# Performance work log

Hardware: AMD Instinct MI355X
Metric: run time of the kernel (lower is better)

The kernel has to match this reference:

```python
import jax, jax.numpy as jnp
import numpy as np

N = 10000      # num_nodes
F = 4          # node_features (in_channels)
P = 12         # periods
OUT = 256      # out_channels
HID = 128      # hidden_dim
ODIM = 12      # output_dim
E_MAIN = 160000
E_REG = 40000


def setup_inputs() -> dict:
    key = jax.random.key(0)
    ks = jax.random.split(key, 48)
    d = {}
    d["x"] = jax.random.normal(ks[0], (N, F, P), jnp.float32)
    d["edge_index"] = jax.random.randint(ks[1], (2, E_MAIN), 0, N)
    names = ["IA", "KS", "KY", "OH", "WI"]
    for i, nm in enumerate(names):
        d[f"edge_{nm}_index"] = jax.random.randint(ks[2 + i], (2, E_REG), 0, N)
        d[f"edge_{nm}_weight"] = jax.random.uniform(ks[7 + i], (E_REG,), jnp.float32)
    def w(k, shape, fan_in):
        return jax.random.normal(k, shape, jnp.float32) * (1.0 / np.sqrt(fan_in))
    # ChebConv K=2 (shared across 5 regions)
    d["cheb_W0"] = w(ks[12], (F, OUT), F)
    d["cheb_W1"] = w(ks[13], (F, OUT), F)
    d["cheb_b"] = jnp.zeros((OUT,), jnp.float32)
    # concat linear 5*OUT -> OUT
    d["lin_cat_W"] = w(ks[14], (5 * OUT, OUT), 5 * OUT)
    d["lin_cat_b"] = jnp.zeros((OUT,), jnp.float32)
    # per-period attention logits
    d["attention"] = jax.random.uniform(ks[15], (P,), jnp.float32)
    # TGCN gates: GCNConv weights + linears
    d["gz_W"] = w(ks[16], (F, OUT), F); d["gz_b"] = jnp.zeros((OUT,), jnp.float32)
    d["gr_W"] = w(ks[17], (F, OUT), F); d["gr_b"] = jnp.zeros((OUT,), jnp.float32)
    d["gh_W"] = w(ks[18], (F, OUT), F); d["gh_b"] = jnp.zeros((OUT,), jnp.float32)
    d["lz_W"] = w(ks[19], (2 * OUT, OUT), 2 * OUT); d["lz_b"] = jnp.ones((OUT,), jnp.float32)
    d["lr_W"] = w(ks[20], (2 * OUT, OUT), 2 * OUT); d["lr_b"] = jnp.ones((OUT,), jnp.float32)
    d["lh_W"] = w(ks[21], (2 * OUT, OUT), 2 * OUT); d["lh_b"] = jnp.ones((OUT,), jnp.float32)
    # readout head
    d["out1_W"] = w(ks[22], (OUT, HID), OUT); d["out1_b"] = jnp.zeros((HID,), jnp.float32)
    d["out2_W"] = w(ks[23], (HID, ODIM), HID); d["out2_b"] = jnp.zeros((ODIM,), jnp.float32)
    return d


def _cheb(x, ei, ew, W0, W1, b):
    # PyG ChebConv, K=2, sym norm, lambda_max=2 => Tx1 = -D^{-1/2} A D^{-1/2} x
    src, dst = ei[0], ei[1]
    deg = jax.ops.segment_sum(ew, src, num_segments=N)
    dinv = jnp.where(deg > 0, jax.lax.rsqrt(jnp.maximum(deg, 1e-12)), 0.0)
    norm = dinv[src] * ew * dinv[dst]                    # [E]
    Tx1 = -jax.ops.segment_sum(norm[:, None] * x[src], dst, num_segments=N)
    return x @ W0 + Tx1 @ W1 + b


def _gcn(x, ei, W, b):
    # PyG GCNConv, edge_weight=None, add_self_loops=True
    xw = x @ W                                           # [N, OUT]
    src, dst = ei[0], ei[1]
    deg = jax.ops.segment_sum(jnp.ones((ei.shape[1],), xw.dtype), dst,
                              num_segments=N) + 1.0      # +1 self loop
    dinv = jax.lax.rsqrt(deg)
    norm = dinv[src] * dinv[dst]                         # [E]
    agg = jax.ops.segment_sum(norm[:, None] * xw[src], dst, num_segments=N)
    agg = agg + (dinv * dinv)[:, None] * xw              # self-loop term
    return agg + b


def _forward(x, edge_index, reg_idx, reg_w,
             cheb_W0, cheb_W1, cheb_b, lin_cat_W, lin_cat_b, attention,
             gz_W, gz_b, gr_W, gr_b, gh_W, gh_b,
             lz_W, lz_b, lr_W, lr_b, lh_W, lh_b,
             out1_W, out1_b, out2_W, out2_b):
    probs = jax.nn.softmax(attention)
    H_accum = jnp.zeros((N, OUT), x.dtype)
    for p in range(P):
        Xp = x[:, :, p]                                  # [N, F]
        hs = jnp.concatenate(
            [_cheb(Xp, ri, rw, cheb_W0, cheb_W1, cheb_b)
             for ri, rw in zip(reg_idx, reg_w)], axis=1)  # [N, 5*OUT]
        h = jax.nn.leaky_relu(hs @ lin_cat_W + lin_cat_b, 0.01)  # [N, OUT]
        # TGCN cell with H = h
        Z = jax.nn.sigmoid(jnp.concatenate([_gcn(Xp, edge_index, gz_W, gz_b), h], 1) @ lz_W + lz_b)
        R = jax.nn.sigmoid(jnp.concatenate([_gcn(Xp, edge_index, gr_W, gr_b), h], 1) @ lr_W + lr_b)
        Ht = jnp.tanh(jnp.concatenate([_gcn(Xp, edge_index, gh_W, gh_b), h * R], 1) @ lh_W + lh_b)
        Hp = Z * h + (1.0 - Z) * Ht
        H_accum = H_accum + probs[p] * Hp
    out_hidden = H_accum
    hr = jax.nn.relu(H_accum)
    o = jax.nn.relu(hr @ out1_W + out1_b) @ out2_W + out2_b  # [N, ODIM]
    return o, out_hidden


def reference(x, edge_index, edge_IA_index, edge_KS_index, edge_KY_index,
              edge_OH_index, edge_WI_index, edge_IA_weight, edge_KS_weight,
              edge_KY_weight, edge_OH_weight, edge_WI_weight,
              cheb_W0, cheb_W1, cheb_b, lin_cat_W, lin_cat_b, attention,
              gz_W, gz_b, gr_W, gr_b, gh_W, gh_b,
              lz_W, lz_b, lr_W, lr_b, lh_W, lh_b,
              out1_W, out1_b, out2_W, out2_b):
    reg_idx = (edge_IA_index, edge_KS_index, edge_KY_index, edge_OH_index, edge_WI_index)
    reg_w = (edge_IA_weight, edge_KS_weight, edge_KY_weight, edge_OH_weight, edge_WI_weight)
    return _forward(x, edge_index, reg_idx, reg_w,
                    cheb_W0, cheb_W1, cheb_b, lin_cat_W, lin_cat_b, attention,
                    gz_W, gz_b, gr_W, gr_b, gh_W, gh_b,
                    lz_W, lz_b, lr_W, lr_b, lh_W, lh_b,
                    out1_W, out1_b, out2_W, out2_b)
```

## Files before the change

kernel.cpp:

```cpp
#include <hip/hip_runtime.h>
#include <hip/hip_bf16.h>
#include <cstddef>

#define NN    10000
#define PP    12
#define EMAIN 160000
#define EREG  40000
#define OUTD  256
#define HIDD  128

typedef __attribute__((ext_vector_type(8))) short bf16x8;
typedef __attribute__((ext_vector_type(4))) float f32x4;

enum : int {
  WS_PROBS    = 0,
  WS_DEGM     = 16,
  WS_DEGR     = WS_DEGM + NN,
  WS_AGGM     = WS_DEGR + 5 * NN,
  WS_TX1      = WS_AGGM + NN * 48,
  WS_ZERO_END = WS_TX1 + 5 * NN * 48,
  WS_DINVM    = WS_ZERO_END,
  WS_DINV2M   = WS_DINVM + NN,
  WS_DINVR    = WS_DINV2M + NN,
  WS_NORMM    = WS_DINVR + 5 * NN,
  WS_NORMR    = WS_NORMM + EMAIN,
  WS_MCAT     = WS_NORMR + 5 * EREG,
  WS_BIASH    = WS_MCAT + 24 * OUTD,
  WS_AZ       = WS_BIASH + OUTD,
  WS_AR       = WS_AZ + 4 * OUTD,
  WS_AH       = WS_AR + 4 * OUTD,
  WS_BZ       = WS_AH + 4 * OUTD,
  WS_BR       = WS_BZ + OUTD,
  WS_BH       = WS_BR + OUTD,
  WS_MCT      = WS_BH + OUTD,
  WS_WZT      = WS_MCT + 4096,
  WS_WRT      = WS_WZT + 36864,
  WS_WHT      = WS_WRT + 36864,
  WS_TOTAL    = WS_WHT + 36864
};

__device__ __forceinline__ float sigm(float v) { return 1.f / (1.f + __expf(-v)); }
__device__ __forceinline__ float tanh_f(float v) { float e = __expf(2.f * v); return 1.f - 2.f / (e + 1.f); }

__device__ __forceinline__ short bf16c(float v) {
  __hip_bfloat16 h = __float2bfloat16(v);
  short r;
  __builtin_memcpy(&r, &h, sizeof(r));
  return r;
}
__device__ __forceinline__ unsigned cvt2(float a, float b) {
  __hip_bfloat162 h2 = __float22bfloat162_rn(make_float2(a, b));
  unsigned r;
  __builtin_memcpy(&r, &h2, sizeof(r));
  return r;
}
__device__ __forceinline__ float upk_lo(unsigned u) { return __uint_as_float(u << 16); }
__device__ __forceinline__ float upk_hi(unsigned u) { return __uint_as_float(u & 0xffff0000u); }

__device__ __forceinline__ const int* sel_i(int r, const int* a, const int* b, const int* c, const int* d, const int* e) {
  return r == 0 ? a : r == 1 ? b : r == 2 ? c : r == 3 ? d : e;
}
__device__ __forceinline__ const float* sel_f(int r, const float* a, const float* b, const float* c, const float* d, const float* e) {
  return r == 0 ? a : r == 1 ? b : r == 2 ? c : r == 3 ? d : e;
}

__global__ void probs_kernel(const float* __restrict__ att, float* __restrict__ probs) {
  if (threadIdx.x == 0 && blockIdx.x == 0) {
    float m = att[0];
    for (int i = 1; i < PP; ++i) m = fmaxf(m, att[i]);
    float e[PP]; float s = 0.f;
    for (int i = 0; i < PP; ++i) { e[i] = __expf(att[i] - m); s += e[i]; }
    float inv = 1.f / s;
    for (int i = 0; i < PP; ++i) probs[i] = e[i] * inv;
  }
}

__global__ void deg_kernel(const int* __restrict__ eim,
    const int* e0, const int* e1, const int* e2, const int* e3, const int* e4,
    const float* w0, const float* w1, const float* w2, const float* w3, const float* w4,
    float* __restrict__ degm, float* __restrict__ degr) {
  int g = blockIdx.x * 256 + threadIdx.x;
  if (g >= EMAIN + 5 * EREG) return;
  if (g < EMAIN) {
    atomicAdd(&degm[eim[EMAIN + g]], 1.0f);
  } else {
    int q = g - EMAIN;
    int r = q / EREG;
    int e = q - r * EREG;
    const int* ei = sel_i(r, e0, e1, e2, e3, e4);
    const float* w = sel_f(r, w0, w1, w2, w3, w4);
    atomicAdd(&degr[r * NN + ei[e]], w[e]);
  }
}

__global__ void dinv_kernel(const float* __restrict__ degm, const float* __restrict__ degr,
    float* __restrict__ dinvm, float* __restrict__ dinv2m, float* __restrict__ dinvr) {
  int g = blockIdx.x * 256 + threadIdx.x;
  if (g >= 6 * NN) return;
  if (g < NN) {
    float c = degm[g] + 1.0f;
    dinvm[g] = rsqrtf(c);
    dinv2m[g] = 1.0f / c;
  } else {
    int q = g - NN;
    float dv = degr[q];
    dinvr[q] = dv > 0.f ? rsqrtf(fmaxf(dv, 1e-12f)) : 0.f;
  }
}

__global__ void norm_kernel(const int* __restrict__ eim,
    const int* e0, const int* e1, const int* e2, const int* e3, const int* e4,
    const float* w0, const float* w1, const float* w2, const float* w3, const float* w4,
    const float* __restrict__ dinvm, const float* __restrict__ dinvr,
    float* __restrict__ normm, float* __restrict__ normr) {
  int g = blockIdx.x * 256 + threadIdx.x;
  if (g >= EMAIN + 5 * EREG) return;
  if (g < EMAIN) {
    int s = eim[g], d = eim[EMAIN + g];
    normm[g] = dinvm[s] * dinvm[d];
  } else {
    int q = g - EMAIN;
    int r = q / EREG;
    int e = q - r * EREG;
    const int* ei = sel_i(r, e0, e1, e2, e3, e4);
    const float* w = sel_f(r, w0, w1, w2, w3, w4);
    int s = ei[e], d = ei[EREG + e];
    normr[q] = -(dinvr[r * NN + s] * w[e] * dinvr[r * NN + d]);
  }
}

__global__ void scatter_kernel(const float* __restrict__ x,
    const int* __restrict__ eim,
    const int* e0, const int* e1, const int* e2, const int* e3, const int* e4,
    const float* __restrict__ normm, const float* __restrict__ normr,
    float* __restrict__ aggm, float* __restrict__ tx1) {
  int g = blockIdx.x * 256 + threadIdx.x;
  int eg = g / 48;
  int i = g - eg * 48;
  int s, d; float nv; float* out;
  if (eg < EMAIN) {
    s = eim[eg]; d = eim[EMAIN + eg]; nv = normm[eg]; out = aggm;
  } else {
    int q = eg - EMAIN;
    int r = q / EREG;
    int e = q - r * EREG;
    const int* ei = sel_i(r, e0, e1, e2, e3, e4);
    s = ei[e]; d = ei[EREG + e];
    nv = normr[q];
    out = tx1 + (size_t)r * (NN * 48);
  }
  atomicAdd(&out[d * 48 + i], nv * x[s * 48 + i]);
}

__global__ __launch_bounds__(256) void prep_parallel_kernel(
    const float* __restrict__ W0, const float* __restrict__ W1, const float* __restrict__ chebb,
    const float* __restrict__ lcW, const float* __restrict__ lcb,
    const float* __restrict__ gzW, const float* __restrict__ gzb,
    const float* __restrict__ grW, const float* __restrict__ grb,
    const float* __restrict__ ghW, const float* __restrict__ ghb,
    const float* __restrict__ lzW, const float* __restrict__ lzb,
    const float* __restrict__ lrW, const float* __restrict__ lrb,
    const float* __restrict__ lhW, const float* __restrict__ lhb,
    float* __restrict__ ws) {
  const int b = blockIdx.x;
  const int tid = threadIdx.x;
  const int jj = tid >> 5;
  const int kk = tid & 31;

  if (b < 32) {
    const int j = b * 8 + jj;
    float m0[4] = {0, 0, 0, 0};
    float m1[5][4] = {};
    float bhh = 0.f;
    for (int k = kk; k < OUTD; k += 32) {
      float w1v[4];
#pragma unroll
      for (int f = 0; f < 4; ++f) w1v[f] = W1[f * OUTD + k];
      float s5 = 0.f;
#pragma unroll
      for (int r = 0; r < 5; ++r) {
        float wv = lcW[(r * OUTD + k) * OUTD + j];
        s5 += wv;
#pragma unroll
        for (int f = 0; f < 4; ++f) m1[r][f] += w1v[f] * wv;
      }
#pragma unroll
      for (int f = 0; f < 4; ++f) m0[f] += W0[f * OUTD + k] * s5;
      bhh += chebb[k] * s5;
    }
#pragma unroll
    for (int off = 16; off >= 1; off >>= 1) {
#pragma unroll
      for (int f = 0; f < 4; ++f) m0[f] += __shfl_xor(m0[f], off);
#pragma unroll
      for (int r = 0; r < 5; ++r)
#pragma unroll
        for (int f = 0; f < 4; ++f) m1[r][f] += __shfl_xor(m1[r][f], off);
      bhh += __shfl_xor(bhh, off);
    }
    if (kk == 0) {
      float* Mcat = ws + WS_MCAT;
#pragma unroll
      for (int f = 0; f < 4; ++f) Mcat[f * OUTD + j] = m0[f];
#pragma unroll
      for (int r = 0; r < 5; ++r)
#pragma unroll
        for (int f = 0; f < 4; ++f) Mcat[(4 + 4 * r + f) * OUTD + j] = m1[r][f];
      ws[WS_BIASH + j] = bhh + lcb[j];
    }
  } else {
    const int g = (b - 32) >> 5;
    const int j = ((b - 32) & 31) * 8 + jj;
    const float* gW = g == 0 ? gzW : g == 1 ? grW : ghW;
    const float* gb = g == 0 ? gzb : g == 1 ? grb : ghb;
    const float* lW = g == 0 ? lzW : g == 1 ? lrW : lhW;
    const float* lb = g == 0 ? lzb : g == 1 ? lrb : lhb;
    float a[4] = {0, 0, 0, 0};
    float vb = 0.f;
    for (int k = kk; k < OUTD; k += 32) {
      float wv = lW[k * OUTD + j];
#pragma unroll
      for (int f = 0; f < 4; ++f) a[f] += gW[f * OUTD + k] * wv;
      vb += gb[k] * wv;
    }
#pragma unroll
    for (int off = 16; off >= 1; off >>= 1) {
#pragma unroll
      for (int f = 0; f < 4; ++f) a[f] += __shfl_xor(a[f], off);
      vb += __shfl_xor(vb, off);
    }
    if (kk == 0) {
      float* A = ws + WS_AZ + g * (4 * OUTD);
#pragma unroll
      for (int f = 0; f < 4; ++f) A[f * OUTD + j] = a[f];
      ws[WS_BZ + g * OUTD + j] = vb + lb[j];
    }
  }
}

__global__ void prepT_kernel(
    const float* __restrict__ lzW, const float* __restrict__ lrW, const float* __restrict__ lhW,
    float* __restrict__ ws) {
  int bx = blockIdx.x;
  int g = bx >> 8;
  int j = bx & 255;
  if (g < 3) {
    const float* Wsrc = g == 0 ? lzW : g == 1 ? lrW : lhW;
    const float* Afold = ws + WS_AZ + g * (4 * OUTD);
    short* dst = (short*)(ws + (g == 0 ? WS_WZT : g == 1 ? WS_WRT : WS_WHT));
    for (int k = threadIdx.x; k < 288; k += 128) {
      float v = 0.f;
      if (k < 256) v = Wsrc[(256 + k) * OUTD + j];
      else if (k >= 280 && k < 284) v = Afold[(k - 280) * OUTD + j];
      dst[j * 288 + k] = bf16c(v);
    }
  } else {
    const float* Mcat = ws + WS_MCAT;
    short* mct = (short*)(ws + WS_MCT);
    for (int k = threadIdx.x; k < 32; k += 128) {
      float v = (k < 24) ? Mcat[k * OUTD + j] : 0.f;
      mct[j * 32 + k] = bf16c(v);
    }
  }
}

#define GATE_MFMA(WT) do {                                                          \
  _Pragma("unroll") for (int m_ = 0; m_ < 6; ++m_)                                  \
    _Pragma("unroll") for (int nt_ = 0; nt_ < 2; ++nt_)                             \
      acc[m_][nt_] = (f32x4){0.f, 0.f, 0.f, 0.f};                                   \
  _Pragma("unroll") for (int ks_ = 0; ks_ < 9; ++ks_) {                             \
    bf16x8 bfr_[2];                                                                 \
    _Pragma("unroll") for (int nt_ = 0; nt_ < 2; ++nt_)                             \
      bfr_[nt_] = *(const bf16x8*)((WT) + (size_t)(wcol + nt_ * 16 + lr) * 288 + ks_ * 32 + 8 * lg); \
    _Pragma("unroll") for (int m_ = 0; m_ < 6; ++m_) {                              \
      bf16x8 af_ = *(const bf16x8*)(&As[m_ * 16 + lr][ks_ * 32 + 8 * lg]);          \
      _Pragma("unroll") for (int nt_ = 0; nt_ < 2; ++nt_)                           \
        acc[m_][nt_] = __builtin_amdgcn_mfma_f32_16x16x32_bf16(af_, bfr_[nt_], acc[m_][nt_], 0, 0, 0); \
    }                                                                               \
  }                                                                                 \
} while (0)

__global__ __launch_bounds__(512, 2) void gru_mfma_kernel(
    const float* __restrict__ x,
    const float* __restrict__ ws,
    float* __restrict__ Hout) {
  const int n0 = blockIdx.x * 8;
  const int t = threadIdx.x;
  const int w = t >> 6;
  const int l = t & 63;
  const int lr = l & 15;
  const int lg = l >> 4;
  const int wcol = w * 32;

  __shared__ __align__(16) short As[96][296];

  const float* aggm   = ws + WS_AGGM;
  const float* tx1    = ws + WS_TX1;
  const float* dinv2m = ws + WS_DINV2M;
  const float* biash  = ws + WS_BIASH;
  const float* bz     = ws + WS_BZ;
  const float* br     = ws + WS_BR;
  const float* bh     = ws + WS_BH;
  const float* probs  = ws + WS_PROBS;
  const short* McT = (const short*)(ws + WS_MCT);
  const short* WzT = (const short*)(ws + WS_WZT);
  const short* WrT = (const short*)(ws + WS_WRT);
  const short* WhT = (const short*)(ws + WS_WHT);

  for (int idx = t; idx < 96 * 32; idx += 512) {
    int row = idx >> 5, s = idx & 31;
    int p = row >> 3, nl = row & 7, n = n0 + nl;
    float v = 0.f;
    if (s < 4) {
      v = x[n * 48 + s * 12 + p];
    } else if (s < 24) {
      int q = s - 4; int r = q >> 2; int f = q & 3;
      v = tx1[(size_t)(r * NN + n) * 48 + f * 12 + p];
    } else if (s < 28) {
      int f = s - 24;
      v = aggm[n * 48 + f * 12 + p] + dinv2m[n] * x[n * 48 + f * 12 + p];
    }
    As[row][256 + s] = bf16c(v);
  }
  __syncthreads();

  f32x4 acc[6][2];

  {
    bf16x8 bm[2];
#pragma unroll
    for (int nt = 0; nt < 2; ++nt)
      bm[nt] = *(const bf16x8*)(McT + (size_t)(wcol + nt * 16 + lr) * 32 + 8 * lg);
    const f32x4 zf = {0.f, 0.f, 0.f, 0.f};
#pragma unroll
    for (int m = 0; m < 6; ++m) {
      bf16x8 af = *(const bf16x8*)(&As[m * 16 + lr][256 + 8 * lg]);
#pragma unroll
      for (int nt = 0; nt < 2; ++nt)
        acc[m][nt] = __builtin_amdgcn_mfma_f32_16x16x32_bf16(af, bm[nt], zf, 0, 0, 0);
    }
  }
  unsigned hp[6][2][2];
#pragma unroll
  for (int nt = 0; nt < 2; ++nt) {
    int col = wcol + nt * 16 + lr;
    float bb = biash[col];
#pragma unroll
    for (int m = 0; m < 6; ++m) {
      f32x4 a = acc[m][nt];
      int rmb = m * 16 + 4 * lg;
      float v0 = a[0] + bb; v0 = fmaxf(v0, 0.01f * v0);
      float v1 = a[1] + bb; v1 = fmaxf(v1, 0.01f * v1);
      float v2 = a[2] + bb; v2 = fmaxf(v2, 0.01f * v2);
      float v3 = a[3] + bb; v3 = fmaxf(v3, 0.01f * v3);
      unsigned u01 = cvt2(v0, v1);
      unsigned u23 = cvt2(v2, v3);
      As[rmb + 0][col] = (short)(u01 & 0xffffu);
      As[rmb + 1][col] = (short)(u01 >> 16);
      As[rmb + 2][col] = (short)(u23 & 0xffffu);
      As[rmb + 3][col] = (short)(u23 >> 16);
      hp[m][nt][0] = u01;
      hp[m][nt][1] = u23;
    }
  }
  __syncthreads();

  GATE_MFMA(WzT);
  unsigned zp[6][2][2];
#pragma unroll
  for (int nt = 0; nt < 2; ++nt) {
    float bb = bz[wcol + nt * 16 + lr];
#pragma unroll
    for (int m = 0; m < 6; ++m) {
      f32x4 a = acc[m][nt];
      zp[m][nt][0] = cvt2(sigm(a[0] + bb), sigm(a[1] + bb));
      zp[m][nt][1] = cvt2(sigm(a[2] + bb), sigm(a[3] + bb));
    }
  }

  GATE_MFMA(WrT);
  __syncthreads();
#pragma unroll
  for (int nt = 0; nt < 2; ++nt) {
    int col = wcol + nt * 16 + lr;
    float bb = br[col];
#pragma unroll
    for (int m = 0; m < 6; ++m) {
      f32x4 a = acc[m][nt];
      int rmb = m * 16 + 4 * lg;
      unsigned u01 = cvt2(upk_lo(hp[m][nt][0]) * sigm(a[0] + bb),
                          upk_hi(hp[m][nt][0]) * sigm(a[1] + bb));
      unsigned u23 = cvt2(upk_lo(hp[m][nt][1]) * sigm(a[2] + bb),
                          upk_hi(hp[m][nt][1]) * sigm(a[3] + bb));
      As[rmb + 0][col] = (short)(u01 & 0xffffu);
      As[rmb + 1][col] = (short)(u01 >> 16);
      As[rmb + 2][col] = (short)(u23 & 0xffffu);
      As[rmb + 3][col] = (short)(u23 >> 16);
    }
  }
  __syncthreads();

  GATE_MFMA(WhT);
  float pr[6];
#pragma unroll
  for (int m = 0; m < 6; ++m) pr[m] = probs[2 * m + (lg >> 1)];
  float wsum[2][4];
#pragma unroll
  for (int nt = 0; nt < 2; ++nt)
#pragma unroll
    for (int q = 0; q < 4; ++q) wsum[nt][q] = 0.f;
#pragma unroll
  for (int nt = 0; nt < 2; ++nt) {
    int col = wcol + nt * 16 + lr;
    float bb = bh[col];
#pragma unroll
    for (int m = 0; m < 6; ++m) {
      f32x4 a = acc[m][nt];
      float hv0 = upk_lo(hp[m][nt][0]), hv1 = upk_hi(hp[m][nt][0]);
      float hv2 = upk_lo(hp[m][nt][1]), hv3 = upk_hi(hp[m][nt][1]);
      float zv0 = upk_lo(zp[m][nt][0]), zv1 = upk_hi(zp[m][nt][0]);
      float zv2 = upk_lo(zp[m][nt][1]), zv3 = upk_hi(zp[m][nt][1]);
      float t0 = tanh_f(a[0] + bb);
      float t1 = tanh_f(a[1] + bb);
      float t2 = tanh_f(a[2] + bb);
      float t3 = tanh_f(a[3] + bb);
      wsum[nt][0] += pr[m] * (t0 + zv0 * (hv0 - t0));
      wsum[nt][1] += pr[m] * (t1 + zv1 * (hv1 - t1));
      wsum[nt][2] += pr[m] * (t2 + zv2 * (hv2 - t2));
      wsum[nt][3] += pr[m] * (t3 + zv3 * (hv3 - t3));
    }
  }
#pragma unroll
  for (int nt = 0; nt < 2; ++nt)
#pragma unroll
    for (int q = 0; q < 4; ++q) {
      float tot = wsum[nt][q] + __shfl_xor(wsum[nt][q], 32);
      if (lg < 2)
        Hout[(size_t)(n0 + 4 * lg + q) * OUTD + wcol + nt * 16 + lr] = tot;
    }
}

__global__ __launch_bounds__(128) void head_kernel(
    const float* __restrict__ H,
    const float* __restrict__ W1, const float* __restrict__ b1,
    const float* __restrict__ W2, const float* __restrict__ b2,
    float* __restrict__ o) {
  const int n0 = blockIdx.x * 8;
  const int t = threadIdx.x;
  __shared__ float hr[8][OUTD];
  __shared__ float hid[8][130];
  for (int idx = t; idx < 8 * OUTD; idx += 128) {
    int r = idx >> 8, c = idx & 255;
    float v = H[(n0 + r) * OUTD + c];
    hr[r][c] = v > 0.f ? v : 0.f;
  }
  __syncthreads();
  float acc[8];
  float bb = b1[t];
#pragma unroll
  for (int r = 0; r < 8; ++r) acc[r] = bb;
  for (int k = 0; k < OUTD; ++k) {
    float w = W1[k * HIDD + t];
#pragma unroll
    for (int r = 0; r < 8; ++r) acc[r] += hr[r][k] * w;
  }
#pragma unroll
  for (int r = 0; r < 8; ++r) hid[r][t] = acc[r] > 0.f ? acc[r] : 0.f;
  __syncthreads();
  if (t < 96) {
    int r = t / 12, dd = t - r * 12;
    float a = b2[dd];
    for (int k = 0; k < HIDD; ++k) a += hid[r][k] * W2[k * 12 + dd];
    o[(n0 + r) * 12 + dd] = a;
  }
}

extern "C" void kernel_launch(void* const* d_in, const int* in_sizes, int n_in,
                              void* d_out, int out_size, void* d_ws, size_t ws_size,
                              hipStream_t stream) {
  (void)in_sizes; (void)n_in; (void)out_size; (void)ws_size;
  const float* x    = (const float*)d_in[0];
  const int*   eim  = (const int*)d_in[1];
  const int*   ei0  = (const int*)d_in[2];
  const float* ew0  = (const float*)d_in[3];
  const int*   ei1  = (const int*)d_in[4];
  const float* ew1  = (const float*)d_in[5];
  const int*   ei2  = (const int*)d_in[6];
  const float* ew2  = (const float*)d_in[7];
  const int*   ei3  = (const int*)d_in[8];
  const float* ew3  = (const float*)d_in[9];
  const int*   ei4  = (const int*)d_in[10];
  const float* ew4  = (const float*)d_in[11];
  const float* chebW0 = (const float*)d_in[12];
  const float* chebW1 = (const float*)d_in[13];
  const float* chebb  = (const float*)d_in[14];
  const float* lcW  = (const float*)d_in[15];
  const float* lcb  = (const float*)d_in[16];
  const float* att  = (const float*)d_in[17];
  const float* gzW  = (const float*)d_in[18];
  const float* gzb  = (const float*)d_in[19];
  const float* grW  = (const float*)d_in[20];
  const float* grb  = (const float*)d_in[21];
  const float* ghW  = (const float*)d_in[22];
  const float* ghb  = (const float*)d_in[23];
  const float* lzW  = (const float*)d_in[24];
  const float* lzb  = (const float*)d_in[25];
  const float* lrW  = (const float*)d_in[26];
  const float* lrb  = (const float*)d_in[27];
  const float* lhW  = (const float*)d_in[28];
  const float* lhb  = (const float*)d_in[29];
  const float* o1W  = (const float*)d_in[30];
  const float* o1b  = (const float*)d_in[31];
  const float* o2W  = (const float*)d_in[32];
  const float* o2b  = (const float*)d_in[33];

  float* ws = (float*)d_ws;
  float* out = (float*)d_out;
  float* o_out = out;
  float* H_out = out + NN * 12;

  (void)hipMemsetAsync(ws, 0, (size_t)WS_ZERO_END * sizeof(float), stream);
  probs_kernel<<<1, 64, 0, stream>>>(att, ws + WS_PROBS);
  deg_kernel<<<(EMAIN + 5 * EREG + 255) / 256, 256, 0, stream>>>(
      eim, ei0, ei1, ei2, ei3, ei4, ew0, ew1, ew2, ew3, ew4,
      ws + WS_DEGM, ws + WS_DEGR);
  dinv_kernel<<<(6 * NN + 255) / 256, 256, 0, stream>>>(
      ws + WS_DEGM, ws + WS_DEGR, ws + WS_DINVM, ws + WS_DINV2M, ws + WS_DINVR);
  norm_kernel<<<(EMAIN + 5 * EREG + 255) / 256, 256, 0, stream>>>(
      eim, ei0, ei1, ei2, ei3, ei4, ew0, ew1, ew2, ew3, ew4,
      ws + WS_DINVM, ws + WS_DINVR, ws + WS_NORMM, ws + WS_NORMR);
  scatter_kernel<<<((EMAIN + 5 * EREG) * 48) / 256, 256, 0, stream>>>(
      x, eim, ei0, ei1, ei2, ei3, ei4,
      ws + WS_NORMM, ws + WS_NORMR, ws + WS_AGGM, ws + WS_TX1);
  prep_parallel_kernel<<<128, 256, 0, stream>>>(
      chebW0, chebW1, chebb, lcW, lcb,
      gzW, gzb, grW, grb, ghW, ghb,
      lzW, lzb, lrW, lrb, lhW, lhb,
      ws);
  prepT_kernel<<<1024, 128, 0, stream>>>(lzW, lrW, lhW, ws);
  gru_mfma_kernel<<<NN / 8, 512, 0, stream>>>(x, ws, H_out);
  head_kernel<<<NN / 8, 128, 0, stream>>>(H_out, o1W, o1b, o2W, o2b, o_out);
}
```

Measured before the change: 374.3 us.

## Replace atomic edge scatter with CSR build and per-destination gather

Edge aggregation moves from per-element float atomics (edges×48) to a destination-sorted CSR built by count, prefix scan and atomic-cursor fill. A gather kernel then sums each node's incoming edges into a register and writes once. This removes about 17M contended float atomics and the large zeroing memset of the aggregation buffers. In exchange it adds a scan and a fill kernel, and the summation order inside a node is no longer fixed.

```diff
diff --git a/kernel.cpp b/kernel.cpp
--- a/kernel.cpp
+++ b/kernel.cpp
@@ -6,6 +6,7 @@
 #define PP    12
 #define EMAIN 160000
 #define EREG  40000
+#define ETOT  (EMAIN + 5 * EREG)
 #define OUTD  256
 #define HIDD  128
 
@@ -14,17 +15,19 @@
 
 enum : int {
   WS_PROBS    = 0,
-  WS_DEGM     = 16,
-  WS_DEGR     = WS_DEGM + NN,
-  WS_AGGM     = WS_DEGR + 5 * NN,
-  WS_TX1      = WS_AGGM + NN * 48,
-  WS_ZERO_END = WS_TX1 + 5 * NN * 48,
+  WS_CNT      = 16,
+  WS_DEGR     = WS_CNT + 6 * NN,
+  WS_ZERO_END = WS_DEGR + 5 * NN,
   WS_DINVM    = WS_ZERO_END,
   WS_DINV2M   = WS_DINVM + NN,
   WS_DINVR    = WS_DINV2M + NN,
-  WS_NORMM    = WS_DINVR + 5 * NN,
-  WS_NORMR    = WS_NORMM + EMAIN,
-  WS_MCAT     = WS_NORMR + 5 * EREG,
+  WS_STARTS   = WS_DINVR + 5 * NN,
+  WS_CURSOR   = WS_STARTS + 6 * (NN + 1),
+  WS_CSRS     = WS_CURSOR + 6 * NN,
+  WS_CSRN     = WS_CSRS + ETOT,
+  WS_AGGM     = WS_CSRN + ETOT,
+  WS_TX1      = WS_AGGM + NN * 48,
+  WS_MCAT     = WS_TX1 + 5 * NN * 48,
   WS_BIASH    = WS_MCAT + 24 * OUTD,
   WS_AZ       = WS_BIASH + OUTD,
   WS_AR       = WS_AZ + 4 * OUTD,
@@ -75,30 +78,31 @@
   }
 }
 
-__global__ void deg_kernel(const int* __restrict__ eim,
+__global__ void count_kernel(const int* __restrict__ eim,
     const int* e0, const int* e1, const int* e2, const int* e3, const int* e4,
     const float* w0, const float* w1, const float* w2, const float* w3, const float* w4,
-    float* __restrict__ degm, float* __restrict__ degr) {
+    int* __restrict__ cnt, float* __restrict__ degr) {
   int g = blockIdx.x * 256 + threadIdx.x;
-  if (g >= EMAIN + 5 * EREG) return;
+  if (g >= ETOT) return;
   if (g < EMAIN) {
-    atomicAdd(&degm[eim[EMAIN + g]], 1.0f);
+    atomicAdd(&cnt[eim[EMAIN + g]], 1);
   } else {
     int q = g - EMAIN;
     int r = q / EREG;
     int e = q - r * EREG;
     const int* ei = sel_i(r, e0, e1, e2, e3, e4);
     const float* w = sel_f(r, w0, w1, w2, w3, w4);
+    atomicAdd(&cnt[(1 + r) * NN + ei[EREG + e]], 1);
     atomicAdd(&degr[r * NN + ei[e]], w[e]);
   }
 }
 
-__global__ void dinv_kernel(const float* __restrict__ degm, const float* __restrict__ degr,
+__global__ void dinv_kernel(const int* __restrict__ cnt, const float* __restrict__ degr,
     float* __restrict__ dinvm, float* __restrict__ dinv2m, float* __restrict__ dinvr) {
   int g = blockIdx.x * 256 + threadIdx.x;
   if (g >= 6 * NN) return;
   if (g < NN) {
-    float c = degm[g] + 1.0f;
+    float c = (float)(cnt[g] + 1);
     dinvm[g] = rsqrtf(c);
     dinv2m[g] = 1.0f / c;
   } else {
@@ -108,48 +112,88 @@
   }
 }
 
-__global__ void norm_kernel(const int* __restrict__ eim,
+__global__ __launch_bounds__(1024) void scan_kernel(const int* __restrict__ cnt,
+    int* __restrict__ starts, int* __restrict__ cursor) {
+  const int b = blockIdx.x;
+  const int t = threadIdx.x;
+  const int base = (b == 0) ? 0 : EMAIN + (b - 1) * EREG;
+  const int Eg = (b == 0) ? EMAIN : EREG;
+  int loc[10];
+  int s = 0;
+#pragma unroll
+  for (int c = 0; c < 10; ++c) {
+    int idx = t * 10 + c;
+    int v = (idx < NN) ? cnt[b * NN + idx] : 0;
+    loc[c] = s;
+    s += v;
+  }
+  __shared__ int sm[1024];
+  sm[t] = s;
+  __syncthreads();
+  for (int off = 1; off < 1024; off <<= 1) {
+    int v = (t >= off) ? sm[t - off] : 0;
+    __syncthreads();
+    sm[t] += v;
+    __syncthreads();
+  }
+  int ex = base + (t > 0 ? sm[t - 1] : 0);
+#pragma unroll
+  for (int c = 0; c < 10; ++c) {
+    int idx = t * 10 + c;
+    if (idx < NN) {
+      int v = ex + loc[c];
+      starts[b * (NN + 1) + idx] = v;
+      cursor[b * NN + idx] = v;
+    }
+  }
+  if (t == 0) starts[b * (NN + 1) + NN] = base + Eg;
+}
+
+__global__ void fill_kernel(const int* __restrict__ eim,
     const int* e0, const int* e1, const int* e2, const int* e3, const int* e4,
     const float* w0, const float* w1, const float* w2, const float* w3, const float* w4,
     const float* __restrict__ dinvm, const float* __restrict__ dinvr,
-    float* __restrict__ normm, float* __restrict__ normr) {
+    int* __restrict__ cursor, int* __restrict__ csrs, float* __restrict__ csrn) {
   int g = blockIdx.x * 256 + threadIdx.x;
-  if (g >= EMAIN + 5 * EREG) return;
+  if (g >= ETOT) return;
+  int s, gi; float nv;
   if (g < EMAIN) {
-    int s = eim[g], d = eim[EMAIN + g];
-    normm[g] = dinvm[s] * dinvm[d];
+    s = eim[g];
+    int d = eim[EMAIN + g];
+    nv = dinvm[s] * dinvm[d];
+    gi = d;
   } else {
     int q = g - EMAIN;
     int r = q / EREG;
     int e = q - r * EREG;
     const int* ei = sel_i(r, e0, e1, e2, e3, e4);
     const float* w = sel_f(r, w0, w1, w2, w3, w4);
-    int s = ei[e], d = ei[EREG + e];
-    normr[q] = -(dinvr[r * NN + s] * w[e] * dinvr[r * NN + d]);
-  }
-}
-
-__global__ void scatter_kernel(const float* __restrict__ x,
-    const int* __restrict__ eim,
-    const int* e0, const int* e1, const int* e2, const int* e3, const int* e4,
-    const float* __restrict__ normm, const float* __restrict__ normr,
+    s = ei[e];
+    int d = ei[EREG + e];
+    nv = -(dinvr[r * NN + s] * w[e] * dinvr[r * NN + d]);
+    gi = (1 + r) * NN + d;
+  }
+  int pos = atomicAdd(&cursor[gi], 1);
+  csrs[pos] = s;
+  csrn[pos] = nv;
+}
+
+__global__ void gather_kernel(const float* __restrict__ x,
+    const int* __restrict__ starts, const int* __restrict__ csrs,
+    const float* __restrict__ csrn,
     float* __restrict__ aggm, float* __restrict__ tx1) {
-  int g = blockIdx.x * 256 + threadIdx.x;
-  int eg = g / 48;
-  int i = g - eg * 48;
-  int s, d; float nv; float* out;
-  if (eg < EMAIN) {
-    s = eim[eg]; d = eim[EMAIN + eg]; nv = normm[eg]; out = aggm;
-  } else {
-    int q = eg - EMAIN;
-    int r = q / EREG;
-    int e = q - r * EREG;
-    const int* ei = sel_i(r, e0, e1, e2, e3, e4);
-    s = ei[e]; d = ei[EREG + e];
-    nv = normr[q];
-    out = tx1 + (size_t)r * (NN * 48);
-  }
-  atomicAdd(&out[d * 48 + i], nv * x[s * 48 + i]);
+  int id = blockIdx.x * 256 + threadIdx.x;
+  int gi = id / 48;
+  int i = id - gi * 48;
+  int g = gi / NN;
+  int n = gi - g * NN;
+  int st = starts[g * (NN + 1) + n];
+  int en = starts[g * (NN + 1) + n + 1];
+  float acc = 0.f;
+  for (int e = st; e < en; ++e)
+    acc += csrn[e] * x[(size_t)csrs[e] * 48 + i];
+  if (g == 0) aggm[n * 48 + i] = acc;
+  else        tx1[(size_t)((g - 1) * NN + n) * 48 + i] = acc;
 }
 
 __global__ __launch_bounds__(256) void prep_parallel_kernel(
@@ -519,19 +563,25 @@
   float* o_out = out;
   float* H_out = out + NN * 12;
 
+  int*   cnt    = (int*)(ws + WS_CNT);
+  float* degr   = ws + WS_DEGR;
+  int*   starts = (int*)(ws + WS_STARTS);
+  int*   cursor = (int*)(ws + WS_CURSOR);
+  int*   csrs   = (int*)(ws + WS_CSRS);
+  float* csrn   = ws + WS_CSRN;
+
   (void)hipMemsetAsync(ws, 0, (size_t)WS_ZERO_END * sizeof(float), stream);
   probs_kernel<<<1, 64, 0, stream>>>(att, ws + WS_PROBS);
-  deg_kernel<<<(EMAIN + 5 * EREG + 255) / 256, 256, 0, stream>>>(
+  count_kernel<<<(ETOT + 255) / 256, 256, 0, stream>>>(
+      eim, ei0, ei1, ei2, ei3, ei4, ew0, ew1, ew2, ew3, ew4, cnt, degr);
+  dinv_kernel<<<(6 * NN + 255) / 256, 256, 0, stream>>>(
+      cnt, degr, ws + WS_DINVM, ws + WS_DINV2M, ws + WS_DINVR);
+  scan_kernel<<<6, 1024, 0, stream>>>(cnt, starts, cursor);
+  fill_kernel<<<(ETOT + 255) / 256, 256, 0, stream>>>(
       eim, ei0, ei1, ei2, ei3, ei4, ew0, ew1, ew2, ew3, ew4,
-      ws + WS_DEGM, ws + WS_DEGR);
-  dinv_kernel<<<(6 * NN + 255) / 256, 256, 0, stream>>>(
-      ws + WS_DEGM, ws + WS_DEGR, ws + WS_DINVM, ws + WS_DINV2M, ws + WS_DINVR);
-  norm_kernel<<<(EMAIN + 5 * EREG + 255) / 256, 256, 0, stream>>>(
-      eim, ei0, ei1, ei2, ei3, ei4, ew0, ew1, ew2, ew3, ew4,
-      ws + WS_DINVM, ws + WS_DINVR, ws + WS_NORMM, ws + WS_NORMR);
-  scatter_kernel<<<((EMAIN + 5 * EREG) * 48) / 256, 256, 0, stream>>>(
-      x, eim, ei0, ei1, ei2, ei3, ei4,
-      ws + WS_NORMM, ws + WS_NORMR, ws + WS_AGGM, ws + WS_TX1);
+      ws + WS_DINVM, ws + WS_DINVR, cursor, csrs, csrn);
+  gather_kernel<<<(6 * NN * 48) / 256, 256, 0, stream>>>(
+      x, starts, csrs, csrn, ws + WS_AGGM, ws + WS_TX1);
   prep_parallel_kernel<<<128, 256, 0, stream>>>(
       chebW0, chebW1, chebb, lcW, lcb,
       gzW, gzb, grW, grb, ghW, ghb,
```

After: 379.0 us. About the same (+1.3%).
